# Kernel tuning notes

Hardware: AMD Instinct MI355X
Metric: run time of the kernel (lower is better)

Reference implementation:

```python
import jax, jax.numpy as jnp
import numpy as np

N_NODES = 10000
N_EDGES = 50000
N_GRAPHS = 64
NODE_DIM = 32
EDGE_DIM = 16
HID = 64
EDGE_HID = 128
OUT_DIM = 1
T_STEPS = 3       # message-passing rounds
S2S_STEPS = 6     # Set2Set processing steps


def setup_inputs() -> dict:
    key = jax.random.key(0)
    ks = jax.random.split(key, 24)
    def w(k, shape, scale):
        return (jax.random.normal(k, shape, dtype=jnp.float32) * scale)
    inp = {}
    inp["node_features"] = jax.random.normal(ks[0], (N_NODES, NODE_DIM), dtype=jnp.float32)
    inp["edge_features"] = jax.random.normal(ks[1], (N_EDGES, EDGE_DIM), dtype=jnp.float32)
    inp["edge_index"] = jax.random.randint(ks[2], (2, N_EDGES), 0, N_NODES, dtype=jnp.int32)
    # sorted, fully-covering graph assignment (nodes of each graph are contiguous)
    inp["batch_indices"] = ((jnp.arange(N_NODES) * N_GRAPHS) // N_NODES).astype(jnp.int32)
    # input projection
    inp["W_proj"] = w(ks[3], (NODE_DIM, HID), 1.0 / np.sqrt(NODE_DIM))
    inp["b_proj"] = jnp.zeros((HID,), jnp.float32)
    # edge network MLP: edge_dim -> edge_hid -> hid*hid
    inp["W_e1"] = w(ks[4], (EDGE_DIM, EDGE_HID), 1.0 / np.sqrt(EDGE_DIM))
    inp["b_e1"] = jnp.zeros((EDGE_HID,), jnp.float32)
    inp["W_e2"] = w(ks[5], (EDGE_HID, HID * HID), 0.01)
    inp["b_e2"] = jnp.zeros((HID * HID,), jnp.float32)
    # GRU cell (torch layout: 3*hid rows = r,z,n)
    inp["W_gih"] = w(ks[6], (3 * HID, HID), 1.0 / np.sqrt(HID))
    inp["W_ghh"] = w(ks[7], (3 * HID, HID), 1.0 / np.sqrt(HID))
    inp["b_gih"] = jnp.zeros((3 * HID,), jnp.float32)
    inp["b_ghh"] = jnp.zeros((3 * HID,), jnp.float32)
    # LSTM cell (torch layout: 4*hid rows = i,f,g,o), input 2*hid
    inp["W_lih"] = w(ks[8], (4 * HID, 2 * HID), 1.0 / np.sqrt(HID))
    inp["W_lhh"] = w(ks[9], (4 * HID, HID), 1.0 / np.sqrt(HID))
    inp["b_lih"] = jnp.zeros((4 * HID,), jnp.float32)
    inp["b_lhh"] = jnp.zeros((4 * HID,), jnp.float32)
    # readout MLP: 2*hid -> hid -> out
    inp["W_m1"] = w(ks[10], (2 * HID, HID), 1.0 / np.sqrt(2 * HID))
    inp["b_m1"] = jnp.zeros((HID,), jnp.float32)
    inp["W_m2"] = w(ks[11], (HID, OUT_DIM), 1.0 / np.sqrt(HID))
    inp["b_m2"] = jnp.zeros((OUT_DIM,), jnp.float32)
    return inp


def _scatter_softmax(e, idx, n_seg):
    mx = jax.ops.segment_max(e, idx, num_segments=n_seg)
    ex = jnp.exp(e - mx[idx])
    s = jax.ops.segment_sum(ex, idx, num_segments=n_seg)
    return ex / (s[idx] + 1e-16)


def _mpnn_forward(node_features, edge_features, edge_index, batch_indices,
                  W_proj, b_proj, W_e1, b_e1, W_e2, b_e2,
                  W_gih, W_ghh, b_gih, b_ghh,
                  W_lih, W_lhh, b_lih, b_lhh,
                  W_m1, b_m1, W_m2, b_m2):
    n_nodes = node_features.shape[0]
    dst = edge_index[0]  # receiving node v
    src = edge_index[1]  # sending node w

    # input projection
    h = node_features @ W_proj + b_proj                       # (N, H)

    # edge network: per-edge transformation matrix A(e_vw) (depends only on edge feats)
    A = jax.nn.relu(edge_features @ W_e1 + b_e1) @ W_e2 + b_e2
    A = A.reshape(-1, HID, HID)                               # (E, H, H)

    # T rounds: gather senders, per-edge bmm, scatter-add to receivers, GRU update
    for _ in range(T_STEPS):
        msgs = jnp.einsum('eij,ej->ei', A, h[src])            # (E, H)
        m = jax.ops.segment_sum(msgs, dst, num_segments=n_nodes)
        gx = m @ W_gih.T + b_gih                              # (N, 3H)
        gh = h @ W_ghh.T + b_ghh
        xr, xz, xn = jnp.split(gx, 3, axis=-1)
        hr, hz, hn = jnp.split(gh, 3, axis=-1)
        r = jax.nn.sigmoid(xr + hr)
        z = jax.nn.sigmoid(xz + hz)
        n = jnp.tanh(xn + r * hn)
        h = (1.0 - z) * n + z * h

    # Set2Set readout
    hs = jnp.zeros((N_GRAPHS, HID), h.dtype)
    cs = jnp.zeros((N_GRAPHS, HID), h.dtype)
    rs = jnp.zeros((N_GRAPHS, HID), h.dtype)
    for _ in range(S2S_STEPS):
        q = hs[batch_indices]                                 # (N, H)
        e = jnp.sum(h * q, axis=-1)                           # (N,)
        a = _scatter_softmax(e, batch_indices, N_GRAPHS)
        rs = jax.ops.segment_sum(a[:, None] * h, batch_indices, num_segments=N_GRAPHS)
        x = jnp.concatenate([hs, rs], axis=-1)                # (G, 2H)
        gates = x @ W_lih.T + b_lih + hs @ W_lhh.T + b_lhh    # (G, 4H)
        i, f, g, o = jnp.split(gates, 4, axis=-1)
        cs = jax.nn.sigmoid(f) * cs + jax.nn.sigmoid(i) * jnp.tanh(g)
        hs = jax.nn.sigmoid(o) * jnp.tanh(cs)
    ge = jnp.concatenate([hs, rs], axis=-1)                   # (G, 2H)
    return jax.nn.relu(ge @ W_m1 + b_m1) @ W_m2 + b_m2        # (G, out)


def reference(node_features, edge_features, edge_index, batch_indices,
              W_proj, b_proj, W_e1, b_e1, W_e2, b_e2,
              W_gih, W_ghh, b_gih, b_ghh,
              W_lih, W_lhh, b_lih, b_lhh,
              W_m1, b_m1, W_m2, b_m2):
    return _mpnn_forward(node_features, edge_features, edge_index, batch_indices,
                         W_proj, b_proj, W_e1, b_e1, W_e2, b_e2,
                         W_gih, W_ghh, b_gih, b_ghh,
                         W_lih, W_lhh, b_lih, b_lhh,
                         W_m1, b_m1, W_m2, b_m2)
```

## Files before the change

### kernel.cpp

```cpp
#include <hip/hip_runtime.h>

#define N_NODES   10000
#define N_EDGES   50000
#define N_GRAPHS  64
#define NODE_DIM  32
#define EDGE_DIM  16
#define HID       64
#define EHID      128
#define T_STEPS   3
#define S2S_STEPS 6

typedef _Float16 half_t;
typedef _Float16 f16x8 __attribute__((ext_vector_type(8)));
typedef float    f32x4 __attribute__((ext_vector_type(4)));

__device__ __forceinline__ float sigf(float x){ return 1.0f/(1.0f + expf(-x)); }

__global__ void k_zero(float* p, int n){
  int i = blockIdx.x*256 + threadIdx.x;
  if (i < n) p[i] = 0.0f;
}

__global__ void k_proj(const float* __restrict__ nf, const float* __restrict__ Wp,
                       const float* __restrict__ bp, float* __restrict__ h){
  int idx = blockIdx.x*256 + threadIdx.x;
  if (idx >= N_NODES*HID) return;
  int n = idx >> 6;
  int c = idx & 63;
  float acc = bp[c];
  const float* row = nf + (size_t)n*NODE_DIM;
  for (int j = 0; j < NODE_DIM; ++j)
    acc = fmaf(row[j], Wp[j*HID + c], acc);
  h[idx] = acc;
}

__global__ void k_tw2(const float* __restrict__ W2, float* __restrict__ Mm){
  int idx = blockIdx.x*256 + threadIdx.x;
  if (idx >= 64*8192) return;
  int j = idx >> 13; int o = idx & 8191; int k = o >> 6; int i = o & 63;
  Mm[idx] = W2[(size_t)k*4096 + i*64 + j];
}

__global__ void k_w2bt(const float* __restrict__ W2, half_t* __restrict__ BT){
  int idx = blockIdx.x*256 + threadIdx.x;
  if (idx >= 512*2*64*8) return;
  int j    = idx & 7;
  int lane = (idx >> 3) & 63;
  int tk   = (idx >> 9) & 1;
  int tn   = idx >> 10;
  int k = tk*32 + ((lane >> 4) << 3) + j;
  int o = tn*16 + (lane & 15);
  BT[idx] = (half_t)W2[(size_t)(o >> 6)*4096 + (o & 63)*64 + k];
}

__global__ void k_h2a(const float* __restrict__ h, half_t* __restrict__ AT){
  int idx = blockIdx.x*256 + threadIdx.x;
  if (idx >= 625*2*64*8) return;
  int j    = idx & 7;
  int lane = (idx >> 3) & 63;
  int tk   = (idx >> 9) & 1;
  int tm   = idx >> 10;
  int mrow = tm*16 + (lane & 15);
  int k    = tk*32 + ((lane >> 4) << 3) + j;
  AT[idx] = (half_t)h[(size_t)mrow*64 + k];
}

__global__ void k_twg(const float* __restrict__ Wg, const float* __restrict__ Wh,
                      float* __restrict__ WgT, float* __restrict__ WhT){
  int idx = blockIdx.x*256 + threadIdx.x;
  if (idx >= 192*64) return;
  int row = idx >> 6;
  int j   = idx & 63;
  WgT[j*192 + row] = Wg[(size_t)row*64 + j];
  WhT[j*192 + row] = Wh[(size_t)row*64 + j];
}

__global__ void k_ehid(const float* __restrict__ ef, const float* __restrict__ W1,
                       const float* __restrict__ b1, float* __restrict__ Hid){
  int idx = blockIdx.x*256 + threadIdx.x;
  if (idx >= N_EDGES*EHID) return;
  int e = idx >> 7, c = idx & 127;
  float acc = b1[c];
  const float* er = ef + (size_t)e*EDGE_DIM;
  for (int j = 0; j < EDGE_DIM; ++j)
    acc = fmaf(er[j], W1[j*EHID + c], acc);
  Hid[idx] = fmaxf(acc, 0.0f);
}

__global__ void k_ehid16(const float* __restrict__ ef, const float* __restrict__ W1,
                         const float* __restrict__ b1, half_t* __restrict__ Hid16){
  int idx = blockIdx.x*256 + threadIdx.x;
  if (idx >= N_EDGES*EHID) return;
  int e = idx >> 7, c = idx & 127;
  float acc = b1[c];
  const float* er = ef + (size_t)e*EDGE_DIM;
  for (int j = 0; j < EDGE_DIM; ++j)
    acc = fmaf(er[j], W1[j*EHID + c], acc);
  Hid16[idx] = (half_t)fmaxf(acc, 0.0f);
}

__global__ void k_bh(const float* __restrict__ h, const float* __restrict__ be2,
                     float* __restrict__ bh){
  int idx = blockIdx.x*256 + threadIdx.x;
  if (idx >= N_NODES*HID) return;
  int n = idx >> 6, i = idx & 63;
  float acc = 0.0f;
  const float* row = be2 + (size_t)i*64;
  const float* hr  = h + (size_t)n*64;
  for (int j = 0; j < 64; ++j)
    acc = fmaf(row[j], hr[j], acc);
  bh[idx] = acc;
}

__global__ void k_hist(const int* __restrict__ ei, int* __restrict__ deg){
  int e = blockIdx.x*256 + threadIdx.x;
  if (e >= N_EDGES) return;
  atomicAdd(&deg[ei[N_EDGES + e]], 1);
}

__global__ void k_scan(const int* __restrict__ deg, int* __restrict__ rowptr,
                       int* __restrict__ cursor){
  __shared__ int part[256];
  int t = threadIdx.x;
  int base = t*40;
  int s = 0;
  for (int i = 0; i < 40; ++i){
    int idx = base + i;
    if (idx < N_NODES) s += deg[idx];
  }
  part[t] = s;
  __syncthreads();
  for (int off = 1; off < 256; off <<= 1){
    int v = (t >= off) ? part[t - off] : 0;
    __syncthreads();
    part[t] += v;
    __syncthreads();
  }
  int run = (t > 0) ? part[t - 1] : 0;
  for (int i = 0; i < 40; ++i){
    int idx = base + i;
    if (idx < N_NODES){
      rowptr[idx] = run;
      cursor[idx] = run;
      run += deg[idx];
    }
  }
  if (t == 255) rowptr[N_NODES] = run;
}

__global__ void k_scatter(const int* __restrict__ ei, int* __restrict__ cursor,
                          int* __restrict__ csr){
  int e = blockIdx.x*256 + threadIdx.x;
  if (e >= N_EDGES) return;
  int src = ei[N_EDGES + e];
  int pos = atomicAdd(&cursor[src], 1);
  csr[pos] = e;
}

__global__ void k_cgemm_mfma(const half_t* __restrict__ AT,
                             const half_t* __restrict__ BT,
                             half_t* __restrict__ C){
  int wv   = threadIdx.x >> 6;
  int lane = threadIdx.x & 63;
  int tm   = blockIdx.x;
  int kt   = blockIdx.y;
  const f16x8* Ab = (const f16x8*)AT + (size_t)tm*128;
  f16x8 a0 = Ab[lane];
  f16x8 a1 = Ab[64 + lane];
  f32x4 acc[4][8];
  #pragma unroll
  for (int is = 0; is < 4; ++is)
    #pragma unroll
    for (int jj = 0; jj < 8; ++jj){
      acc[is][jj][0]=0.f; acc[is][jj][1]=0.f; acc[is][jj][2]=0.f; acc[is][jj][3]=0.f;
    }
  #pragma unroll
  for (int jj = 0; jj < 8; ++jj){
    int ke = kt*32 + wv*8 + jj;
    const f16x8* Bb = (const f16x8*)BT + (size_t)(ke*4)*128 + lane;
    #pragma unroll
    for (int is = 0; is < 4; ++is){
      f16x8 b0 = Bb[is*128];
      f16x8 b1 = Bb[is*128 + 64];
      acc[is][jj] = __builtin_amdgcn_mfma_f32_16x16x32_f16(a0, b0, acc[is][jj], 0, 0, 0);
      acc[is][jj] = __builtin_amdgcn_mfma_f32_16x16x32_f16(a1, b1, acc[is][jj], 0, 0, 0);
    }
  }
  int quad = lane >> 4;
  int colb = lane & 15;
  #pragma unroll
  for (int r = 0; r < 4; ++r){
    int n = tm*16 + quad*4 + r;
    #pragma unroll
    for (int is = 0; is < 4; ++is){
      f16x8 v;
      #pragma unroll
      for (int jj = 0; jj < 8; ++jj) v[jj] = (half_t)acc[is][jj][r];
      *(f16x8*)&C[(size_t)n*8192 + kt*2048 + is*512 + (size_t)(wv*16 + colb)*8] = v;
    }
  }
}

__global__ void k_cgemm(const float* __restrict__ h, const float* __restrict__ Mm,
                        half_t* __restrict__ C, int lo, int hi){
  __shared__ float hs[16][64];
  int n0 = lo + blockIdx.x*16;
  int o0 = blockIdx.y*256 + threadIdx.x;
  for (int idx = threadIdx.x; idx < 16*64; idx += 256){
    int nn = idx >> 6, j = idx & 63;
    int node = n0 + nn;
    hs[nn][j] = (node < hi) ? h[(size_t)node*64 + j] : 0.0f;
  }
  __syncthreads();
  float acc0[16], acc1[16];
  #pragma unroll
  for (int nn = 0; nn < 16; ++nn){ acc0[nn] = 0.0f; acc1[nn] = 0.0f; }
  for (int j4 = 0; j4 < 16; ++j4){
    const float* M0 = Mm + (size_t)(j4*4)*8192;
    float a0 = M0[o0],            b0 = M0[o0 + 4096];
    float a1 = M0[8192 + o0],     b1 = M0[8192 + o0 + 4096];
    float a2 = M0[2*8192 + o0],   b2 = M0[2*8192 + o0 + 4096];
    float a3 = M0[3*8192 + o0],   b3 = M0[3*8192 + o0 + 4096];
    #pragma unroll
    for (int nn = 0; nn < 16; ++nn){
      float4 hv = *(const float4*)&hs[nn][j4*4];
      acc0[nn] = fmaf(hv.x, a0, acc0[nn]);
      acc1[nn] = fmaf(hv.x, b0, acc1[nn]);
      acc0[nn] = fmaf(hv.y, a1, acc0[nn]);
      acc1[nn] = fmaf(hv.y, b1, acc1[nn]);
      acc0[nn] = fmaf(hv.z, a2, acc0[nn]);
      acc1[nn] = fmaf(hv.z, b2, acc1[nn]);
      acc0[nn] = fmaf(hv.w, a3, acc0[nn]);
      acc1[nn] = fmaf(hv.w, b3, acc1[nn]);
    }
  }
  #pragma unroll
  for (int nn = 0; nn < 16; ++nn){
    int node = n0 + nn;
    if (node < hi){
      half_t* Cr = C + (size_t)(node - lo)*8192;
      Cr[o0]        = (half_t)acc0[nn];
      Cr[o0 + 4096] = (half_t)acc1[nn];
    }
  }
}

__global__ void MPNN_55705725829535_kernel(const int* __restrict__ rowptr,
                                           const int* __restrict__ csr,
                                           const int* __restrict__ ei,
                                           const half_t* __restrict__ Hid16,
                                           const half_t* __restrict__ C,
                                           const float* __restrict__ bh,
                                           float* __restrict__ m){
  __shared__ int dstL[4][16];
  int wave = threadIdx.x >> 6;
  int lane = threadIdx.x & 63;
  int s = blockIdx.x*4 + wave;
  if (s >= N_NODES) return;
  int beg  = rowptr[s];
  int endp = rowptr[s + 1];
  if (beg == endp) return;
  int quad = lane >> 4;
  int colb = lane & 15;
  const f16x8* Cb = (const f16x8*)(C + (size_t)s*8192) + lane;
  f16x8 B[4][4];
  #pragma unroll
  for (int kt = 0; kt < 4; ++kt)
    #pragma unroll
    for (int is = 0; is < 4; ++is)
      B[kt][is] = Cb[kt*256 + is*64];
  float bhc[4];
  #pragma unroll
  for (int is = 0; is < 4; ++is)
    bhc[is] = bh[(size_t)s*64 + is*16 + colb];
  for (int gbeg = beg; gbeg < endp; gbeg += 16){
    int gn = endp - gbeg; if (gn > 16) gn = 16;
    if (lane < 16)
      dstL[wave][lane] = (lane < gn) ? ei[csr[gbeg + lane]] : -1;
    f16x8 A[4];
    if (colb < gn){
      int e = csr[gbeg + colb];
      const f16x8* Hb = (const f16x8*)(Hid16 + (size_t)e*128) + quad;
      #pragma unroll
      for (int kt = 0; kt < 4; ++kt)
        A[kt] = Hb[kt*4];
    } else {
      #pragma unroll
      for (int kt = 0; kt < 4; ++kt)
        #pragma unroll
        for (int q = 0; q < 8; ++q) A[kt][q] = (half_t)0;
    }
    f32x4 acc[4];
    #pragma unroll
    for (int is = 0; is < 4; ++is){
      acc[is][0]=0.f; acc[is][1]=0.f; acc[is][2]=0.f; acc[is][3]=0.f;
    }
    #pragma unroll
    for (int kt = 0; kt < 4; ++kt)
      #pragma unroll
      for (int is = 0; is < 4; ++is)
        acc[is] = __builtin_amdgcn_mfma_f32_16x16x32_f16(A[kt], B[kt][is], acc[is], 0, 0, 0);
    #pragma unroll
    for (int r = 0; r < 4; ++r){
      int jrow = quad*4 + r;
      if (jrow < gn){
        int d = dstL[wave][jrow];
        float* mr = m + (size_t)d*64 + colb;
        #pragma unroll
        for (int is = 0; is < 4; ++is)
          atomicAdd(mr + is*16, acc[is][r] + bhc[is]);
      }
    }
  }
}

__global__ void k_msg_csr(const int* __restrict__ rowptr,
                          const int* __restrict__ csr,
                          const int* __restrict__ ei,
                          const float* __restrict__ Hid,
                          const half_t* __restrict__ C,
                          const float* __restrict__ bh,
                          float* __restrict__ m, int lo, int hi){
  __shared__ float hidL[4][8][128];
  int wave = threadIdx.x >> 6;
  int lane = threadIdx.x & 63;
  int s = lo + blockIdx.x*4 + wave;
  if (s >= hi) return;
  int beg = rowptr[s];
  int endp = rowptr[s + 1];
  if (beg == endp) return;
  float bhv = bh[(size_t)s*64 + lane];
  const half_t* Cb = C + (size_t)(s - lo)*8192 + lane;
  float (*hl)[128] = hidL[wave];
  for (int gbeg = beg; gbeg < endp; gbeg += 8){
    int gn = endp - gbeg; if (gn > 8) gn = 8;
    int dsts[8];
    int e0 = csr[gbeg];
    #pragma unroll
    for (int j = 0; j < 8; ++j){
      int e = (j < gn) ? csr[gbeg + j] : e0;
      dsts[j] = ei[e];
      hl[j][lane]      = Hid[(size_t)e*128 + lane];
      hl[j][lane + 64] = Hid[(size_t)e*128 + 64 + lane];
    }
    float acc[8];
    #pragma unroll
    for (int j = 0; j < 8; ++j) acc[j] = 0.0f;
    #pragma unroll 4
    for (int k = 0; k < 128; ++k){
      float c = (float)Cb[k*64];
      #pragma unroll
      for (int j = 0; j < 8; ++j)
        acc[j] = fmaf(hl[j][k], c, acc[j]);
    }
    for (int j = 0; j < gn; ++j)
      atomicAdd(&m[(size_t)dsts[j]*64 + lane], acc[j] + bhv);
  }
}

__global__ void k_msg_fb(const int* __restrict__ ei, const float* __restrict__ ef,
                         const float* __restrict__ W1, const float* __restrict__ b1,
                         const float* __restrict__ W2, const float* __restrict__ be2,
                         const float* __restrict__ h, float* __restrict__ m){
  __shared__ float HidL[EHID];
  __shared__ __align__(16) float hsL[HID];
  int e = blockIdx.x;
  int t = threadIdx.x;
  int src = ei[N_EDGES + e];
  int dst = ei[e];
  {
    float a0 = b1[t];
    float a1 = b1[t + 64];
    const float* er = ef + (size_t)e*EDGE_DIM;
    for (int j = 0; j < EDGE_DIM; ++j){
      float ev = er[j];
      a0 = fmaf(ev, W1[j*EHID + t],      a0);
      a1 = fmaf(ev, W1[j*EHID + t + 64], a1);
    }
    HidL[t]      = fmaxf(a0, 0.0f);
    HidL[t + 64] = fmaxf(a1, 0.0f);
    hsL[t] = h[(size_t)src*64 + t];
  }
  __syncthreads();
  float acc = 0.0f;
  for (int k = 0; k < EHID; ++k){
    float s = HidL[k];
    if (s != 0.0f){
      const float* w = W2 + (size_t)k*4096 + t*64;
      float partial = 0.0f;
      for (int j = 0; j < 64; ++j)
        partial = fmaf(hsL[j], w[j], partial);
      acc = fmaf(s, partial, acc);
    }
  }
  {
    const float* w = be2 + (size_t)t*64;
    for (int j = 0; j < 64; ++j)
      acc = fmaf(hsL[j], w[j], acc);
  }
  atomicAdd(&m[(size_t)dst*64 + t], acc);
}

__global__ void k_gru(float* __restrict__ h, const float* __restrict__ m,
                      const float* __restrict__ WgT, const float* __restrict__ WhT,
                      const float* __restrict__ bg, const float* __restrict__ bhb){
  __shared__ float mld[16][64];
  __shared__ float hld[16][64];
  int t  = threadIdx.x;
  int i  = t & 63;
  int wv = t >> 6;
  int n0 = blockIdx.x*16;
  for (int idx = t; idx < 16*64; idx += 256){
    int nn = idx >> 6, j = idx & 63;
    int node = n0 + nn;
    mld[nn][j] = m[(size_t)node*64 + j];
    hld[nn][j] = h[(size_t)node*64 + j];
  }
  __syncthreads();
  float xr[4], xz[4], xn[4], hr[4], hz[4], hn[4];
  #pragma unroll
  for (int c = 0; c < 4; ++c){
    xr[c] = bg[i];  xz[c] = bg[64 + i];  xn[c] = bg[128 + i];
    hr[c] = bhb[i]; hz[c] = bhb[64 + i]; hn[c] = bhb[128 + i];
  }
  for (int j = 0; j < 64; ++j){
    const float* wg = WgT + j*192;
    const float* wh = WhT + j*192;
    float wgr = wg[i], wgz = wg[64 + i], wgn = wg[128 + i];
    float whr = wh[i], whz = wh[64 + i], whn = wh[128 + i];
    #pragma unroll
    for (int c = 0; c < 4; ++c){
      int nn = wv*4 + c;
      float mj = mld[nn][j];
      float hj = hld[nn][j];
      xr[c] = fmaf(mj, wgr, xr[c]);
      xz[c] = fmaf(mj, wgz, xz[c]);
      xn[c] = fmaf(mj, wgn, xn[c]);
      hr[c] = fmaf(hj, whr, hr[c]);
      hz[c] = fmaf(hj, whz, hz[c]);
      hn[c] = fmaf(hj, whn, hn[c]);
    }
  }
  #pragma unroll
  for (int c = 0; c < 4; ++c){
    int nn = wv*4 + c;
    float r  = sigf(xr[c] + hr[c]);
    float z  = sigf(xz[c] + hz[c]);
    float nv = tanhf(xn[c] + r*hn[c]);
    h[(size_t)(n0 + nn)*64 + i] = (1.0f - z)*nv + z*hld[nn][i];
  }
}

__global__ void k_s2s(const float* __restrict__ h,
                      const float* __restrict__ Wli, const float* __restrict__ Wlh,
                      const float* __restrict__ bli, const float* __restrict__ blh,
                      const float* __restrict__ Wm1, const float* __restrict__ bm1,
                      const float* __restrict__ Wm2, const float* __restrict__ bm2,
                      float* __restrict__ out){
  __shared__ float hc[157*65];
  __shared__ float ea[160];
  __shared__ float x[192];
  __shared__ float gpart[512];
  __shared__ float rsp[8][64];
  __shared__ float wredA[8];
  __shared__ float wredB[8];
  __shared__ float hsb[64];
  __shared__ float csb[64];
  __shared__ float rsb[64];
  int g = blockIdx.x;
  int t = threadIdx.x;
  int lane = t & 63;
  int wv   = t >> 6;
  int start = (g*N_NODES + 63) >> 6;
  int end   = ((g + 1)*N_NODES + 63) >> 6;
  int cnt = end - start;
  const float* hg = h + (size_t)start*64;
  for (int idx = t; idx < cnt*64; idx += 512)
    hc[(idx >> 6)*65 + (idx & 63)] = hg[idx];
  if (t < 64){ hsb[t] = 0.0f; csb[t] = 0.0f; rsb[t] = 0.0f; }
  __syncthreads();
  for (int step = 0; step < S2S_STEPS; ++step){
    float ev = -1e30f;
    if (t < cnt){
      float a = 0.0f;
      const float* hr = &hc[t*65];
      for (int i = 0; i < 64; ++i) a = fmaf(hr[i], hsb[i], a);
      ev = a;
    }
    float v = ev;
    for (int o = 32; o > 0; o >>= 1) v = fmaxf(v, __shfl_xor(v, o));
    if (lane == 0) wredA[wv] = v;
    __syncthreads();
    float mx = wredA[0];
    #pragma unroll
    for (int i = 1; i < 8; ++i) mx = fmaxf(mx, wredA[i]);
    float ex = (t < cnt) ? expf(ev - mx) : 0.0f;
    float sv = ex;
    for (int o = 32; o > 0; o >>= 1) sv += __shfl_xor(sv, o);
    if (lane == 0) wredB[wv] = sv;
    __syncthreads();
    float ssum = 0.0f;
    #pragma unroll
    for (int i = 0; i < 8; ++i) ssum += wredB[i];
    if (t < cnt) ea[t] = ex / (ssum + 1e-16f);
    __syncthreads();
    {
      int n0 = wv*20;
      int n1 = n0 + 20; if (n1 > cnt) n1 = cnt;
      float r = 0.0f;
      for (int n = n0; n < n1; ++n)
        r = fmaf(ea[n], hc[n*65 + lane], r);
      rsp[wv][lane] = r;
    }
    __syncthreads();
    if (t < 64){
      float r = rsp[0][t] + rsp[1][t] + rsp[2][t] + rsp[3][t]
              + rsp[4][t] + rsp[5][t] + rsp[6][t] + rsp[7][t];
      rsb[t] = r;
      x[t]        = hsb[t];
      x[64 + t]   = r;
      x[128 + t]  = hsb[t];
    }
    __syncthreads();
    {
      int gate = t & 255;
      int half = t >> 8;
      float gl = 0.0f;
      if (half == 0){
        const float* wr = Wli + (size_t)gate*128;
        for (int jj = 0; jj < 96; ++jj) gl = fmaf(x[jj], wr[jj], gl);
      } else {
        const float* wr = Wli + (size_t)gate*128;
        for (int jj = 96; jj < 128; ++jj) gl = fmaf(x[jj], wr[jj], gl);
        const float* wh = Wlh + (size_t)gate*64;
        for (int jj = 0; jj < 64; ++jj) gl = fmaf(x[128 + jj], wh[jj], gl);
      }
      gpart[t] = gl;
    }
    __syncthreads();
    if (t < 64){
      float iv = sigf (gpart[t]       + gpart[t + 256]       + bli[t]       + blh[t]);
      float fv = sigf (gpart[64 + t]  + gpart[64 + t + 256]  + bli[64 + t]  + blh[64 + t]);
      float gv = tanhf(gpart[128 + t] + gpart[128 + t + 256] + bli[128 + t] + blh[128 + t]);
      float ov = sigf (gpart[192 + t] + gpart[192 + t + 256] + bli[192 + t] + blh[192 + t]);
      float c  = fv*csb[t] + iv*gv;
      csb[t] = c;
      hsb[t] = ov*tanhf(c);
    }
    __syncthreads();
  }
  float rv = 0.0f;
  if (t < 64){
    float v = bm1[t];
    for (int j = 0; j < 64; ++j) v = fmaf(hsb[j], Wm1[(size_t)j*64 + t],        v);
    for (int j = 0; j < 64; ++j) v = fmaf(rsb[j], Wm1[(size_t)(64 + j)*64 + t], v);
    v = fmaxf(v, 0.0f);
    rv = v * Wm2[t];
  }
  for (int o = 32; o > 0; o >>= 1) rv += __shfl_xor(rv, o);
  if (lane == 0) wredA[wv] = rv;
  __syncthreads();
  if (t == 0) out[g] = wredA[0] + wredA[1] + wredA[2] + wredA[3]
                     + wredA[4] + wredA[5] + wredA[6] + wredA[7] + bm2[0];
}

extern "C" void kernel_launch(void* const* d_in, const int* in_sizes, int n_in,
                              void* d_out, int out_size, void* d_ws, size_t ws_size,
                              hipStream_t stream){
  (void)in_sizes; (void)n_in; (void)out_size;

  const float* nf  = (const float*)d_in[0];
  const float* ef  = (const float*)d_in[1];
  const int*   ei  = (const int*)d_in[2];
  const float* Wp  = (const float*)d_in[4];
  const float* bp  = (const float*)d_in[5];
  const float* We1 = (const float*)d_in[6];
  const float* be1 = (const float*)d_in[7];
  const float* We2 = (const float*)d_in[8];
  const float* be2 = (const float*)d_in[9];
  const float* Wg  = (const float*)d_in[10];
  const float* Wh  = (const float*)d_in[11];
  const float* bg  = (const float*)d_in[12];
  const float* bhb = (const float*)d_in[13];
  const float* Wli = (const float*)d_in[14];
  const float* Wlh = (const float*)d_in[15];
  const float* bli = (const float*)d_in[16];
  const float* blh = (const float*)d_in[17];
  const float* Wm1 = (const float*)d_in[18];
  const float* bm1 = (const float*)d_in[19];
  const float* Wm2 = (const float*)d_in[20];
  const float* bm2 = (const float*)d_in[21];

  float* out = (float*)d_out;
  float* ws  = (float*)d_ws;

  float* h    = ws;
  float* m    = ws + 640000;
  float* bh   = ws + 1280000;
  float* Mm   = ws + 1920000;
  float* WgT  = ws + 2444288;
  float* WhT  = ws + 2456576;
  float* Hid  = ws + 2468864;
  half_t* Hid16 = (half_t*)Hid;
  int*   deg    = (int*)(ws + 8868864);
  int*   rowptr = deg + 10000;
  int*   cursor = rowptr + 10001;
  int*   csr    = cursor + 10000;
  half_t* AT  = (half_t*)(ws + 8948880);
  half_t* BT  = (half_t*)(ws + 9268880);
  const size_t C_OFF = 9531024;
  half_t* C   = (half_t*)(ws + C_OFF);

  long long c_halves = ((long long)ws_size - (long long)C_OFF*4) / 2;
  int NC = (c_halves > 0) ? (int)(c_halves / 8192) : 0;
  if (NC > N_NODES) NC = N_NODES;
  int use_c_path = (NC >= 512);
  int use_mfma   = (NC >= N_NODES);

  k_proj<<<(N_NODES*HID + 255)/256, 256, 0, stream>>>(nf, Wp, bp, h);

  if (use_c_path){
    k_twg <<<(192*64 + 255)/256, 256, 0, stream>>>(Wg, Wh, WgT, WhT);
    k_zero<<<(10000 + 255)/256, 256, 0, stream>>>((float*)deg, 10000);
    k_hist<<<(N_EDGES + 255)/256, 256, 0, stream>>>(ei, deg);
    k_scan<<<1, 256, 0, stream>>>(deg, rowptr, cursor);
    k_scatter<<<(N_EDGES + 255)/256, 256, 0, stream>>>(ei, cursor, csr);
    if (use_mfma){
      k_ehid16<<<(N_EDGES*EHID + 255)/256, 256, 0, stream>>>(ef, We1, be1, Hid16);
      k_w2bt<<<(512*2*64*8 + 255)/256, 256, 0, stream>>>(We2, BT);
      for (int step = 0; step < T_STEPS; ++step){
        k_zero<<<(N_NODES*HID + 255)/256, 256, 0, stream>>>(m, N_NODES*HID);
        k_bh<<<(N_NODES*HID + 255)/256, 256, 0, stream>>>(h, be2, bh);
        k_h2a<<<(625*2*64*8 + 255)/256, 256, 0, stream>>>(h, AT);
        dim3 grid(625, 4);
        k_cgemm_mfma<<<grid, 256, 0, stream>>>(AT, BT, C);
        MPNN_55705725829535_kernel<<<(N_NODES + 3)/4, 256, 0, stream>>>(
            rowptr, csr, ei, Hid16, C, bh, m);
        k_gru<<<625, 256, 0, stream>>>(h, m, WgT, WhT, bg, bhb);
      }
    } else {
      k_ehid<<<(N_EDGES*EHID + 255)/256, 256, 0, stream>>>(ef, We1, be1, Hid);
      k_tw2<<<(64*8192)/256, 256, 0, stream>>>(We2, Mm);
      for (int step = 0; step < T_STEPS; ++step){
        k_zero<<<(N_NODES*HID + 255)/256, 256, 0, stream>>>(m, N_NODES*HID);
        k_bh<<<(N_NODES*HID + 255)/256, 256, 0, stream>>>(h, be2, bh);
        for (int lo = 0; lo < N_NODES; lo += NC){
          int hi = (lo + NC < N_NODES) ? lo + NC : N_NODES;
          int cnt = hi - lo;
          dim3 grid((cnt + 15)/16, 16);
          k_cgemm<<<grid, 256, 0, stream>>>(h, Mm, C, lo, hi);
          k_msg_csr<<<(cnt + 3)/4, 256, 0, stream>>>(
              rowptr, csr, ei, Hid, C, bh, m, lo, hi);
        }
        k_gru<<<625, 256, 0, stream>>>(h, m, WgT, WhT, bg, bhb);
      }
    }
  } else {
    k_twg <<<(192*64 + 255)/256, 256, 0, stream>>>(Wg, Wh, WgT, WhT);
    for (int step = 0; step < T_STEPS; ++step){
      k_zero<<<(N_NODES*HID + 255)/256, 256, 0, stream>>>(m, N_NODES*HID);
      k_msg_fb<<<N_EDGES, 64, 0, stream>>>(ei, ef, We1, be1, We2, be2, h, m);
      k_gru<<<625, 256, 0, stream>>>(h, m, WgT, WhT, bg, bhb);
    }
  }
  k_s2s<<<N_GRAPHS, 512, 0, stream>>>(h, Wli, Wlh, bli, blh,
                                      Wm1, bm1, Wm2, bm2, out);
}
```

Measured before the change: 613.8 us.

## Fuse per-node weight GEMM into edge message kernel via shared memory

Merges the MFMA GEMM that builds per-node 64x64 edge-network matrices into the message-passing kernel, keeping each 16-node tile's matrix slice in LDS instead of writing the full fp16 C buffer to global memory and reading it back. The grid is split by output quarter, so each block computes one quarter of the output columns for 16 nodes and then runs the edge MFMA and atomic scatter for those nodes. This removes a large global write/read per step, but repeats the edge gathers once per quarter and uses large LDS per block, which limits occupancy.

```diff
diff --git a/kernel.cpp b/kernel.cpp
--- a/kernel.cpp
+++ b/kernel.cpp
@@ -157,46 +157,93 @@
   csr[pos] = e;
 }
 
-__global__ void k_cgemm_mfma(const half_t* __restrict__ AT,
-                             const half_t* __restrict__ BT,
-                             half_t* __restrict__ C){
+__global__ void MPNN_55705725829535_kernel(const half_t* __restrict__ AT,
+                                           const half_t* __restrict__ BT,
+                                           const int* __restrict__ rowptr,
+                                           const int* __restrict__ csr,
+                                           const int* __restrict__ ei,
+                                           const half_t* __restrict__ Hid16,
+                                           const float* __restrict__ bh,
+                                           float* __restrict__ m){
+  __shared__ half_t Ct[16][4][520];
+  __shared__ int dstW[4][16];
   int wv   = threadIdx.x >> 6;
   int lane = threadIdx.x & 63;
-  int tm   = blockIdx.x;
-  int kt   = blockIdx.y;
+  int quad = lane >> 4;
+  int colb = lane & 15;
+  int tm = blockIdx.x;
+  int q  = blockIdx.y;
+
   const f16x8* Ab = (const f16x8*)AT + (size_t)tm*128;
   f16x8 a0 = Ab[lane];
   f16x8 a1 = Ab[64 + lane];
-  f32x4 acc[4][8];
   #pragma unroll
-  for (int is = 0; is < 4; ++is)
+  for (int kt = 0; kt < 4; ++kt){
+    f32x4 acc[8];
     #pragma unroll
     for (int jj = 0; jj < 8; ++jj){
-      acc[is][jj][0]=0.f; acc[is][jj][1]=0.f; acc[is][jj][2]=0.f; acc[is][jj][3]=0.f;
-    }
-  #pragma unroll
-  for (int jj = 0; jj < 8; ++jj){
-    int ke = kt*32 + wv*8 + jj;
-    const f16x8* Bb = (const f16x8*)BT + (size_t)(ke*4)*128 + lane;
-    #pragma unroll
-    for (int is = 0; is < 4; ++is){
-      f16x8 b0 = Bb[is*128];
-      f16x8 b1 = Bb[is*128 + 64];
-      acc[is][jj] = __builtin_amdgcn_mfma_f32_16x16x32_f16(a0, b0, acc[is][jj], 0, 0, 0);
-      acc[is][jj] = __builtin_amdgcn_mfma_f32_16x16x32_f16(a1, b1, acc[is][jj], 0, 0, 0);
-    }
-  }
-  int quad = lane >> 4;
-  int colb = lane & 15;
-  #pragma unroll
-  for (int r = 0; r < 4; ++r){
-    int n = tm*16 + quad*4 + r;
-    #pragma unroll
-    for (int is = 0; is < 4; ++is){
+      acc[jj][0]=0.f; acc[jj][1]=0.f; acc[jj][2]=0.f; acc[jj][3]=0.f;
+    }
+    #pragma unroll
+    for (int jj = 0; jj < 8; ++jj){
+      int ke = kt*32 + wv*8 + jj;
+      int tn = ke*4 + q;
+      const f16x8* Bb = (const f16x8*)BT + (size_t)tn*128;
+      acc[jj] = __builtin_amdgcn_mfma_f32_16x16x32_f16(a0, Bb[lane],      acc[jj], 0, 0, 0);
+      acc[jj] = __builtin_amdgcn_mfma_f32_16x16x32_f16(a1, Bb[64 + lane], acc[jj], 0, 0, 0);
+    }
+    #pragma unroll
+    for (int r = 0; r < 4; ++r){
+      int node = quad*4 + r;
       f16x8 v;
       #pragma unroll
-      for (int jj = 0; jj < 8; ++jj) v[jj] = (half_t)acc[is][jj][r];
-      *(f16x8*)&C[(size_t)n*8192 + kt*2048 + is*512 + (size_t)(wv*16 + colb)*8] = v;
+      for (int jj = 0; jj < 8; ++jj) v[jj] = (half_t)acc[jj][r];
+      *(f16x8*)&Ct[node][kt][(wv*16 + colb)*8] = v;
+    }
+  }
+  __syncthreads();
+
+  for (int c = 0; c < 4; ++c){
+    int node = wv*4 + c;
+    int s = tm*16 + node;
+    int beg  = rowptr[s];
+    int endp = rowptr[s + 1];
+    if (beg == endp) continue;
+    f16x8 B[4];
+    #pragma unroll
+    for (int kt = 0; kt < 4; ++kt)
+      B[kt] = *(const f16x8*)&Ct[node][kt][lane*8];
+    float bhc = bh[(size_t)s*64 + q*16 + colb];
+    for (int gbeg = beg; gbeg < endp; gbeg += 16){
+      int gn = endp - gbeg; if (gn > 16) gn = 16;
+      if (lane < 16)
+        dstW[wv][lane] = (lane < gn) ? ei[csr[gbeg + lane]] : -1;
+      f16x8 A[4];
+      if (colb < gn){
+        int e = csr[gbeg + colb];
+        const f16x8* Hb = (const f16x8*)(Hid16 + (size_t)e*128) + quad;
+        #pragma unroll
+        for (int kt = 0; kt < 4; ++kt)
+          A[kt] = Hb[kt*4];
+      } else {
+        #pragma unroll
+        for (int kt = 0; kt < 4; ++kt)
+          #pragma unroll
+          for (int p = 0; p < 8; ++p) A[kt][p] = (half_t)0;
+      }
+      f32x4 acc;
+      acc[0]=0.f; acc[1]=0.f; acc[2]=0.f; acc[3]=0.f;
+      #pragma unroll
+      for (int kt = 0; kt < 4; ++kt)
+        acc = __builtin_amdgcn_mfma_f32_16x16x32_f16(A[kt], B[kt], acc, 0, 0, 0);
+      #pragma unroll
+      for (int r = 0; r < 4; ++r){
+        int jrow = quad*4 + r;
+        if (jrow < gn){
+          int d = dstW[wv][jrow];
+          atomicAdd(&m[(size_t)d*64 + q*16 + colb], acc[r] + bhc);
+        }
+      }
     }
   }
 }
@@ -241,75 +288,6 @@
       half_t* Cr = C + (size_t)(node - lo)*8192;
       Cr[o0]        = (half_t)acc0[nn];
       Cr[o0 + 4096] = (half_t)acc1[nn];
-    }
-  }
-}
-
-__global__ void MPNN_55705725829535_kernel(const int* __restrict__ rowptr,
-                                           const int* __restrict__ csr,
-                                           const int* __restrict__ ei,
-                                           const half_t* __restrict__ Hid16,
-                                           const half_t* __restrict__ C,
-                                           const float* __restrict__ bh,
-                                           float* __restrict__ m){
-  __shared__ int dstL[4][16];
-  int wave = threadIdx.x >> 6;
-  int lane = threadIdx.x & 63;
-  int s = blockIdx.x*4 + wave;
-  if (s >= N_NODES) return;
-  int beg  = rowptr[s];
-  int endp = rowptr[s + 1];
-  if (beg == endp) return;
-  int quad = lane >> 4;
-  int colb = lane & 15;
-  const f16x8* Cb = (const f16x8*)(C + (size_t)s*8192) + lane;
-  f16x8 B[4][4];
-  #pragma unroll
-  for (int kt = 0; kt < 4; ++kt)
-    #pragma unroll
-    for (int is = 0; is < 4; ++is)
-      B[kt][is] = Cb[kt*256 + is*64];
-  float bhc[4];
-  #pragma unroll
-  for (int is = 0; is < 4; ++is)
-    bhc[is] = bh[(size_t)s*64 + is*16 + colb];
-  for (int gbeg = beg; gbeg < endp; gbeg += 16){
-    int gn = endp - gbeg; if (gn > 16) gn = 16;
-    if (lane < 16)
-      dstL[wave][lane] = (lane < gn) ? ei[csr[gbeg + lane]] : -1;
-    f16x8 A[4];
-    if (colb < gn){
-      int e = csr[gbeg + colb];
-      const f16x8* Hb = (const f16x8*)(Hid16 + (size_t)e*128) + quad;
-      #pragma unroll
-      for (int kt = 0; kt < 4; ++kt)
-        A[kt] = Hb[kt*4];
-    } else {
-      #pragma unroll
-      for (int kt = 0; kt < 4; ++kt)
-        #pragma unroll
-        for (int q = 0; q < 8; ++q) A[kt][q] = (half_t)0;
-    }
-    f32x4 acc[4];
-    #pragma unroll
-    for (int is = 0; is < 4; ++is){
-      acc[is][0]=0.f; acc[is][1]=0.f; acc[is][2]=0.f; acc[is][3]=0.f;
-    }
-    #pragma unroll
-    for (int kt = 0; kt < 4; ++kt)
-      #pragma unroll
-      for (int is = 0; is < 4; ++is)
-        acc[is] = __builtin_amdgcn_mfma_f32_16x16x32_f16(A[kt], B[kt][is], acc[is], 0, 0, 0);
-    #pragma unroll
-    for (int r = 0; r < 4; ++r){
-      int jrow = quad*4 + r;
-      if (jrow < gn){
-        int d = dstL[wave][jrow];
-        float* mr = m + (size_t)d*64 + colb;
-        #pragma unroll
-        for (int is = 0; is < 4; ++is)
-          atomicAdd(mr + is*16, acc[is][r] + bhc[is]);
-      }
     }
   }
 }
@@ -633,9 +611,8 @@
         k_bh<<<(N_NODES*HID + 255)/256, 256, 0, stream>>>(h, be2, bh);
         k_h2a<<<(625*2*64*8 + 255)/256, 256, 0, stream>>>(h, AT);
         dim3 grid(625, 4);
-        k_cgemm_mfma<<<grid, 256, 0, stream>>>(AT, BT, C);
-        MPNN_55705725829535_kernel<<<(N_NODES + 3)/4, 256, 0, stream>>>(
-            rowptr, csr, ei, Hid16, C, bh, m);
+        MPNN_55705725829535_kernel<<<grid, 256, 0, stream>>>(
+            AT, BT, rowptr, csr, ei, Hid16, bh, m);
         k_gru<<<625, 256, 0, stream>>>(h, m, WgT, WhT, bg, bhb);
       }
     } else {
```

Measured after the change: 601.2 us. -2.1%, faster.
